# Kernel tuning notes

Measured on AMD Instinct MI355X. Metric: run time of the kernel, lower is better.

## Reference

```python
import jax, jax.numpy as jnp
import numpy as np

TAU_FF = 10
TAU_FB = 10
NB_FF = 8
NB_FB = 1
MU = 0.5
N_IN = 2048
N_HID = 2048
N_OUT = 2048


def raised_cosine_pillow_08(tau, n_basis, mu):
    # Pillow et al. 2008 log-raised-cosine basis; returns [n_basis, tau].
    # Fixed (non-learned) constant in the original module.
    t = jnp.arange(tau, dtype=jnp.float32)
    c = jnp.arange(n_basis, dtype=jnp.float32)
    arg = jnp.clip(mu * jnp.pi * jnp.log1p(t)[None, :] - mu * jnp.pi * c[:, None],
                   -jnp.pi, jnp.pi)
    return 0.5 * (1.0 + jnp.cos(arg))


# transposed like the torch module: [tau, n_basis]
FF_FILT = raised_cosine_pillow_08(TAU_FF, NB_FF, MU).T
FB_FILT = raised_cosine_pillow_08(TAU_FB, NB_FB, MU).T


def _layer_step(inp_hist, spk_hist, ff_w, fb_w, bias, key):
    # inp_hist: [n_in, T]; spk_hist: [n_out, Th]; ff_w: [n_out, n_in, NB_FF]
    T = inp_hist.shape[-1]
    ff_trace = jnp.matmul(inp_hist[..., ::-1], FF_FILT[:T])       # [n_in, NB_FF]
    ff_pot = jnp.einsum('oib,ib->o', ff_w, ff_trace)              # [n_out]
    Th = spk_hist.shape[-1]
    fb_trace = jnp.matmul(spk_hist[:, ::-1], FB_FILT[:Th])        # [n_out, NB_FB]
    fb_pot = jnp.sum(fb_w * fb_trace, axis=-1)                    # [n_out]
    p = jax.nn.sigmoid(ff_pot + fb_pot + bias)
    spikes = jax.random.bernoulli(key, jax.lax.stop_gradient(p)).astype(p.dtype)
    # memory_length (10) > current history width (2), so the update just
    # appends one column (matches torch slice [:, 1-memory_length:]).
    new_hist = jnp.concatenate([spk_hist, spikes[:, None]], axis=-1)
    return p, spikes, new_hist


def setup_inputs() -> dict:
    key = jax.random.key(0)
    ks = jax.random.split(key, 10)

    def xav(k, shape, fan_in, fan_out):
        a = np.sqrt(3.0) * np.sqrt(2.0 / float(fan_in + fan_out))
        return jax.random.uniform(k, shape, jnp.float32, -a, a)

    fi, fo = N_IN * NB_FF, N_HID * NB_FF  # fan of ff_weights [n_out, n_in, nb]
    return {
        'inputs_history': (jax.random.uniform(ks[0], (N_IN, TAU_FF)) < 0.3).astype(jnp.float32),
        'ff_w0': xav(ks[1], (N_HID, N_IN, NB_FF), fi, fo),
        'fb_w0': xav(ks[2], (N_HID, NB_FB), fi, fo),
        'b0': xav(ks[3], (N_HID,), fi, fo),
        'ff_w1': xav(ks[4], (N_HID, N_HID, NB_FF), fi, fo),
        'fb_w1': xav(ks[5], (N_HID, NB_FB), fi, fo),
        'b1': xav(ks[6], (N_HID,), fi, fo),
        'ff_w2': xav(ks[7], (N_OUT, N_HID, NB_FF), fi, fo),
        'fb_w2': xav(ks[8], (N_OUT, NB_FB), fi, fo),
        'b2': xav(ks[9], (N_OUT,), fi, fo),
    }


def reference(inputs_history, ff_w0, fb_w0, b0, ff_w1, fb_w1, b1,
              ff_w2, fb_w2, b2):
    # LayeredSNN.forward with n_samples=1, target=None.
    k0, k1, k2 = jax.random.split(jax.random.key(42), 3)
    h0 = jnp.zeros((N_HID, 2), jnp.float32)   # initial spiking histories
    h1 = jnp.zeros((N_HID, 2), jnp.float32)
    h2 = jnp.zeros((N_OUT, 2), jnp.float32)
    p0, s0, h0 = _layer_step(inputs_history, h0, ff_w0, fb_w0, b0, k0)
    p1, s1, h1 = _layer_step(h0, h1, ff_w1, fb_w1, b1, k1)   # reads updated h0
    p2, s2, h2 = _layer_step(h1, h2, ff_w2, fb_w2, b2, k2)   # out layer
    net_probas = p2[None]                      # [1, n_out]
    net_outputs = s2[None]                     # [1, n_out]
    probas_hidden = jnp.stack([p0, p1])[None]  # [1, n_hidden_layers, n_hid]
    outputs_hidden = jnp.stack([s0, s1])[None]
    return net_probas, net_outputs, probas_hidden, outputs_hidden
```

## Files before the change

kernel.cpp:

```cpp
#include <hip/hip_runtime.h>
#include <hip/hip_bf16.h>
#include <stdint.h>
#include <stddef.h>

#define WS_F_OFF      64
#define WS_TRACE0_OFF 768
#define WS_S0_OFF     131840
#define WS_S1_OFF     148224

__host__ __device__ inline void tf2x32(uint32_t k0, uint32_t k1,
                                       uint32_t& x0, uint32_t& x1) {
  uint32_t ks0 = k0, ks1 = k1, ks2 = k0 ^ k1 ^ 0x1BD11BDAu;
  x0 += ks0; x1 += ks1;
#define TF_ROT(v, n) (((v) << (n)) | ((v) >> (32 - (n))))
#define TF_R(r) { x0 += x1; x1 = TF_ROT(x1, r); x1 ^= x0; }
  TF_R(13) TF_R(15) TF_R(26) TF_R(6)   x0 += ks1; x1 += ks2 + 1u;
  TF_R(17) TF_R(29) TF_R(16) TF_R(24)  x0 += ks2; x1 += ks0 + 2u;
  TF_R(13) TF_R(15) TF_R(26) TF_R(6)   x0 += ks0; x1 += ks1 + 3u;
  TF_R(17) TF_R(29) TF_R(16) TF_R(24)  x0 += ks1; x1 += ks2 + 4u;
  TF_R(13) TF_R(15) TF_R(26) TF_R(6)   x0 += ks2; x1 += ks0 + 5u;
#undef TF_R
#undef TF_ROT
}

__device__ inline double bf2d(unsigned short b) {
  return (double)__uint_as_float(((uint32_t)b) << 16);
}
__device__ inline unsigned short f2bf(float f) {
  uint32_t u = __float_as_uint(f);
  u += 0x7FFFu + ((u >> 16) & 1u);
  return (unsigned short)(u >> 16);
}

__global__ void snn_init_kernel(const uint32_t* __restrict__ x_words,
                                uint8_t* __restrict__ ws) {
  uint32_t* flag = (uint32_t*)ws;
  double* F = (double*)(ws + WS_F_OFF);
  int t = threadIdx.x;
  if (t == 0) {
    int cnt = 0;
    for (int k = 0; k < 256; ++k) {
      uint32_t w = x_words[k];
      cnt += (w == 0u || w == 0x3F800000u) ? 1 : 0;
    }
    *flag = (cnt == 256) ? 0u : 1u;
  }
  if (t < 80) {
    int tt = t >> 3, b = t & 7;
    const double PI = 3.14159265358979311599796346854;
    double arg = 0.5 * PI * log1p((double)tt) - 0.5 * PI * (double)b;
    arg = fmin(fmax(arg, -PI), PI);
    F[t] = 0.5 * (1.0 + cos(arg));
  }
}

__global__ void snn_trace0_kernel(const void* __restrict__ X,
                                  uint8_t* __restrict__ ws) {
  const uint32_t flag = *(const uint32_t*)ws;
  const double* F = (const double*)(ws + WS_F_OFF);
  double* tr = (double*)(ws + WS_TRACE0_OFF);
  int idx = blockIdx.x * blockDim.x + threadIdx.x;
  if (idx >= 2048 * 8) return;
  int i = idx >> 3, b = idx & 7;
  double acc = 0.0;
  if (flag) {
    const unsigned short* Xb = (const unsigned short*)X;
    #pragma unroll
    for (int t = 0; t < 10; ++t) acc += bf2d(Xb[i * 10 + (9 - t)]) * F[t * 8 + b];
  } else {
    const float* Xf = (const float*)X;
    #pragma unroll
    for (int t = 0; t < 10; ++t) acc += (double)Xf[i * 10 + (9 - t)] * F[t * 8 + b];
  }
  tr[idx] = acc;
}

__global__ __launch_bounds__(256) void snn_layer_kernel(
    const void* __restrict__ W, const void* __restrict__ bias,
    uint8_t* __restrict__ ws,
    int traceMode,
    const double* __restrict__ sPrev,
    double* __restrict__ sOutD,
    uint32_t key0, uint32_t key1,
    void* __restrict__ out, int pOff, int sOff)
{
  const uint32_t flag = *(const uint32_t*)ws;
  const double* F = (const double*)(ws + WS_F_OFF);
  const double* tr0 = (const double*)(ws + WS_TRACE0_OFF);
  const int o = blockIdx.x;
  const int tid = threadIdx.x;
  double acc = 0.0;

  if (traceMode == 0) {
    if (flag) {
      const unsigned short* Wrow = (const unsigned short*)W + (size_t)o * 16384;
      for (int i = tid; i < 2048; i += 256) {
        uint4 v = *(const uint4*)(Wrow + i * 8);
        const double* tr = tr0 + i * 8;
        acc += bf2d((unsigned short)(v.x & 0xFFFFu)) * tr[0]
             + bf2d((unsigned short)(v.x >> 16))     * tr[1]
             + bf2d((unsigned short)(v.y & 0xFFFFu)) * tr[2]
             + bf2d((unsigned short)(v.y >> 16))     * tr[3]
             + bf2d((unsigned short)(v.z & 0xFFFFu)) * tr[4]
             + bf2d((unsigned short)(v.z >> 16))     * tr[5]
             + bf2d((unsigned short)(v.w & 0xFFFFu)) * tr[6]
             + bf2d((unsigned short)(v.w >> 16))     * tr[7];
      }
    } else {
      const float* Wrow = (const float*)W + (size_t)o * 16384;
      for (int i = tid; i < 2048; i += 256) {
        float4 a = *(const float4*)(Wrow + i * 8);
        float4 b = *(const float4*)(Wrow + i * 8 + 4);
        const double* tr = tr0 + i * 8;
        acc += (double)a.x * tr[0] + (double)a.y * tr[1]
             + (double)a.z * tr[2] + (double)a.w * tr[3]
             + (double)b.x * tr[4] + (double)b.y * tr[5]
             + (double)b.z * tr[6] + (double)b.w * tr[7];
      }
    }
  } else {
    double F0[8];
    #pragma unroll
    for (int b = 0; b < 8; ++b) F0[b] = F[b];
    if (flag) {
      const unsigned short* Wrow = (const unsigned short*)W + (size_t)o * 16384;
      for (int i = tid; i < 2048; i += 256) {
        double si = sPrev[i];
        uint4 v = *(const uint4*)(Wrow + i * 8);
        double dot = bf2d((unsigned short)(v.x & 0xFFFFu)) * F0[0]
                   + bf2d((unsigned short)(v.x >> 16))     * F0[1]
                   + bf2d((unsigned short)(v.y & 0xFFFFu)) * F0[2]
                   + bf2d((unsigned short)(v.y >> 16))     * F0[3]
                   + bf2d((unsigned short)(v.z & 0xFFFFu)) * F0[4]
                   + bf2d((unsigned short)(v.z >> 16))     * F0[5]
                   + bf2d((unsigned short)(v.w & 0xFFFFu)) * F0[6]
                   + bf2d((unsigned short)(v.w >> 16))     * F0[7];
        acc += si * dot;
      }
    } else {
      const float* Wrow = (const float*)W + (size_t)o * 16384;
      for (int i = tid; i < 2048; i += 256) {
        double si = sPrev[i];
        float4 a = *(const float4*)(Wrow + i * 8);
        float4 b = *(const float4*)(Wrow + i * 8 + 4);
        double dot = (double)a.x * F0[0] + (double)a.y * F0[1]
                   + (double)a.z * F0[2] + (double)a.w * F0[3]
                   + (double)b.x * F0[4] + (double)b.y * F0[5]
                   + (double)b.z * F0[6] + (double)b.w * F0[7];
        acc += si * dot;
      }
    }
  }

  __shared__ double red[256];
  red[tid] = acc;
  __syncthreads();
  for (int s = 128; s > 0; s >>= 1) {
    if (tid < s) red[tid] += red[tid + s];
    __syncthreads();
  }

  if (tid == 0) {
    double bb = flag ? bf2d(((const unsigned short*)bias)[o])
                     : (double)((const float*)bias)[o];
    double x = red[0] + bb;
    double p = 1.0 / (1.0 + exp(-x));
    uint32_t x0 = 0u, x1 = (uint32_t)o;
    tf2x32(key0, key1, x0, x1);
    uint32_t wbits = x0 ^ x1;
    float u = __uint_as_float((wbits >> 9) | 0x3F800000u) - 1.0f;
    double s = ((double)u < p) ? 1.0 : 0.0;
    if (flag) {
      unsigned short* ob = (unsigned short*)out;
      ob[pOff + o] = f2bf((float)p);
      ob[sOff + o] = f2bf((float)s);
    } else {
      float* of = (float*)out;
      of[pOff + o] = (float)p;
      of[sOff + o] = (float)s;
    }
    if (sOutD) sOutD[o] = s;
  }
}

extern "C" void kernel_launch(void* const* d_in, const int* in_sizes, int n_in,
                              void* d_out, int out_size, void* d_ws, size_t ws_size,
                              hipStream_t stream) {
  uint32_t k0a = 0u, k0b = 0u;  tf2x32(0u, 42u, k0a, k0b);
  uint32_t k1a = 0u, k1b = 1u;  tf2x32(0u, 42u, k1a, k1b);
  uint32_t k2a = 0u, k2b = 2u;  tf2x32(0u, 42u, k2a, k2b);

  uint8_t* ws = (uint8_t*)d_ws;
  double* s0d = (double*)(ws + WS_S0_OFF);
  double* s1d = (double*)(ws + WS_S1_OFF);

  snn_init_kernel<<<1, 128, 0, stream>>>((const uint32_t*)d_in[0], ws);
  snn_trace0_kernel<<<64, 256, 0, stream>>>(d_in[0], ws);
  snn_layer_kernel<<<2048, 256, 0, stream>>>(d_in[1], d_in[3], ws, 0, nullptr, s0d,
                                             k0a, k0b, d_out, 4096, 8192);
  snn_layer_kernel<<<2048, 256, 0, stream>>>(d_in[4], d_in[6], ws, 1, s0d, s1d,
                                             k1a, k1b, d_out, 6144, 10240);
  snn_layer_kernel<<<2048, 256, 0, stream>>>(d_in[7], d_in[9], ws, 1, s1d, nullptr,
                                             k2a, k2b, d_out, 0, 2048);
}
```

Baseline: 387.1 us.

## Assign one wavefront per output row and fuse init with trace kernel

```diff
diff --git a/kernel.cpp b/kernel.cpp
--- a/kernel.cpp
+++ b/kernel.cpp
@@ -32,52 +32,57 @@
   return (unsigned short)(u >> 16);
 }
 
-__global__ void snn_init_kernel(const uint32_t* __restrict__ x_words,
-                                uint8_t* __restrict__ ws) {
-  uint32_t* flag = (uint32_t*)ws;
-  double* F = (double*)(ws + WS_F_OFF);
-  int t = threadIdx.x;
-  if (t == 0) {
-    int cnt = 0;
-    for (int k = 0; k < 256; ++k) {
-      uint32_t w = x_words[k];
-      cnt += (w == 0u || w == 0x3F800000u) ? 1 : 0;
-    }
-    *flag = (cnt == 256) ? 0u : 1u;
-  }
-  if (t < 80) {
-    int tt = t >> 3, b = t & 7;
+__global__ __launch_bounds__(256) void snn_prep_kernel(
+    const void* __restrict__ X, uint8_t* __restrict__ ws) {
+  __shared__ unsigned long long smask[4];
+  __shared__ double sF[80];
+  __shared__ int s_flag;
+  const int tid = threadIdx.x;
+
+  const uint32_t* xw = (const uint32_t*)X;
+  uint32_t w = xw[tid];
+  bool ok = (w == 0u || w == 0x3F800000u);
+  unsigned long long m = __ballot(ok);
+  if ((tid & 63) == 0) smask[tid >> 6] = m;
+
+  if (tid < 80) {
+    int tt = tid >> 3, b = tid & 7;
     const double PI = 3.14159265358979311599796346854;
     double arg = 0.5 * PI * log1p((double)tt) - 0.5 * PI * (double)b;
     arg = fmin(fmax(arg, -PI), PI);
-    F[t] = 0.5 * (1.0 + cos(arg));
-  }
-}
-
-__global__ void snn_trace0_kernel(const void* __restrict__ X,
-                                  uint8_t* __restrict__ ws) {
-  const uint32_t flag = *(const uint32_t*)ws;
-  const double* F = (const double*)(ws + WS_F_OFF);
-  double* tr = (double*)(ws + WS_TRACE0_OFF);
-  int idx = blockIdx.x * blockDim.x + threadIdx.x;
-  if (idx >= 2048 * 8) return;
-  int i = idx >> 3, b = idx & 7;
+    sF[tid] = 0.5 * (1.0 + cos(arg));
+  }
+  __syncthreads();
+  if (tid == 0) {
+    bool allbin = ((smask[0] & smask[1] & smask[2] & smask[3]) == ~0ull);
+    s_flag = allbin ? 0 : 1;
+  }
+  __syncthreads();
+  const int flag = s_flag;
+
+  if (blockIdx.x == 0) {
+    if (tid == 0) *(uint32_t*)ws = (uint32_t)flag;
+    if (tid < 80) ((double*)(ws + WS_F_OFF))[tid] = sF[tid];
+  }
+
+  const int idx = blockIdx.x * 256 + tid;
+  const int i = idx >> 3, b = idx & 7;
   double acc = 0.0;
   if (flag) {
     const unsigned short* Xb = (const unsigned short*)X;
     #pragma unroll
-    for (int t = 0; t < 10; ++t) acc += bf2d(Xb[i * 10 + (9 - t)]) * F[t * 8 + b];
+    for (int t = 0; t < 10; ++t) acc += bf2d(Xb[i * 10 + (9 - t)]) * sF[t * 8 + b];
   } else {
     const float* Xf = (const float*)X;
     #pragma unroll
-    for (int t = 0; t < 10; ++t) acc += (double)Xf[i * 10 + (9 - t)] * F[t * 8 + b];
-  }
-  tr[idx] = acc;
+    for (int t = 0; t < 10; ++t) acc += (double)Xf[i * 10 + (9 - t)] * sF[t * 8 + b];
+  }
+  ((double*)(ws + WS_TRACE0_OFF))[idx] = acc;
 }
 
 __global__ __launch_bounds__(256) void snn_layer_kernel(
     const void* __restrict__ W, const void* __restrict__ bias,
-    uint8_t* __restrict__ ws,
+    const uint8_t* __restrict__ ws,
     int traceMode,
     const double* __restrict__ sPrev,
     double* __restrict__ sOutD,
@@ -87,35 +92,42 @@
   const uint32_t flag = *(const uint32_t*)ws;
   const double* F = (const double*)(ws + WS_F_OFF);
   const double* tr0 = (const double*)(ws + WS_TRACE0_OFF);
-  const int o = blockIdx.x;
-  const int tid = threadIdx.x;
-  double acc = 0.0;
+  const int lane = threadIdx.x & 63;
+  const int row = blockIdx.x * 4 + (threadIdx.x >> 6);
+
+  double acc[8];
+  #pragma unroll
+  for (int b = 0; b < 8; ++b) acc[b] = 0.0;
 
   if (traceMode == 0) {
     if (flag) {
-      const unsigned short* Wrow = (const unsigned short*)W + (size_t)o * 16384;
-      for (int i = tid; i < 2048; i += 256) {
-        uint4 v = *(const uint4*)(Wrow + i * 8);
-        const double* tr = tr0 + i * 8;
-        acc += bf2d((unsigned short)(v.x & 0xFFFFu)) * tr[0]
-             + bf2d((unsigned short)(v.x >> 16))     * tr[1]
-             + bf2d((unsigned short)(v.y & 0xFFFFu)) * tr[2]
-             + bf2d((unsigned short)(v.y >> 16))     * tr[3]
-             + bf2d((unsigned short)(v.z & 0xFFFFu)) * tr[4]
-             + bf2d((unsigned short)(v.z >> 16))     * tr[5]
-             + bf2d((unsigned short)(v.w & 0xFFFFu)) * tr[6]
-             + bf2d((unsigned short)(v.w >> 16))     * tr[7];
+      const unsigned short* Wr = (const unsigned short*)W + (size_t)row * 16384;
+      for (int s = 0; s < 32; ++s) {
+        int i = s * 64 + lane;
+        uint4 v = *(const uint4*)(Wr + i * 8);
+        const double2* t = (const double2*)(tr0 + i * 8);
+        double2 t0 = t[0], t1 = t[1], t2 = t[2], t3 = t[3];
+        acc[0] += bf2d((unsigned short)(v.x & 0xFFFFu)) * t0.x;
+        acc[1] += bf2d((unsigned short)(v.x >> 16))     * t0.y;
+        acc[2] += bf2d((unsigned short)(v.y & 0xFFFFu)) * t1.x;
+        acc[3] += bf2d((unsigned short)(v.y >> 16))     * t1.y;
+        acc[4] += bf2d((unsigned short)(v.z & 0xFFFFu)) * t2.x;
+        acc[5] += bf2d((unsigned short)(v.z >> 16))     * t2.y;
+        acc[6] += bf2d((unsigned short)(v.w & 0xFFFFu)) * t3.x;
+        acc[7] += bf2d((unsigned short)(v.w >> 16))     * t3.y;
       }
     } else {
-      const float* Wrow = (const float*)W + (size_t)o * 16384;
-      for (int i = tid; i < 2048; i += 256) {
-        float4 a = *(const float4*)(Wrow + i * 8);
-        float4 b = *(const float4*)(Wrow + i * 8 + 4);
-        const double* tr = tr0 + i * 8;
-        acc += (double)a.x * tr[0] + (double)a.y * tr[1]
-             + (double)a.z * tr[2] + (double)a.w * tr[3]
-             + (double)b.x * tr[4] + (double)b.y * tr[5]
-             + (double)b.z * tr[6] + (double)b.w * tr[7];
+      const float* Wr = (const float*)W + (size_t)row * 16384;
+      for (int s = 0; s < 32; ++s) {
+        int i = s * 64 + lane;
+        float4 a = *(const float4*)(Wr + i * 8);
+        float4 c = *(const float4*)(Wr + i * 8 + 4);
+        const double2* t = (const double2*)(tr0 + i * 8);
+        double2 t0 = t[0], t1 = t[1], t2 = t[2], t3 = t[3];
+        acc[0] += (double)a.x * t0.x;  acc[1] += (double)a.y * t0.y;
+        acc[2] += (double)a.z * t1.x;  acc[3] += (double)a.w * t1.y;
+        acc[4] += (double)c.x * t2.x;  acc[5] += (double)c.y * t2.y;
+        acc[6] += (double)c.z * t3.x;  acc[7] += (double)c.w * t3.y;
       }
     }
   } else {
@@ -123,63 +135,64 @@
     #pragma unroll
     for (int b = 0; b < 8; ++b) F0[b] = F[b];
     if (flag) {
-      const unsigned short* Wrow = (const unsigned short*)W + (size_t)o * 16384;
-      for (int i = tid; i < 2048; i += 256) {
+      const unsigned short* Wr = (const unsigned short*)W + (size_t)row * 16384;
+      for (int s = 0; s < 32; ++s) {
+        int i = s * 64 + lane;
+        uint4 v = *(const uint4*)(Wr + i * 8);
         double si = sPrev[i];
-        uint4 v = *(const uint4*)(Wrow + i * 8);
-        double dot = bf2d((unsigned short)(v.x & 0xFFFFu)) * F0[0]
-                   + bf2d((unsigned short)(v.x >> 16))     * F0[1]
-                   + bf2d((unsigned short)(v.y & 0xFFFFu)) * F0[2]
-                   + bf2d((unsigned short)(v.y >> 16))     * F0[3]
-                   + bf2d((unsigned short)(v.z & 0xFFFFu)) * F0[4]
-                   + bf2d((unsigned short)(v.z >> 16))     * F0[5]
-                   + bf2d((unsigned short)(v.w & 0xFFFFu)) * F0[6]
-                   + bf2d((unsigned short)(v.w >> 16))     * F0[7];
-        acc += si * dot;
+        acc[0] += (bf2d((unsigned short)(v.x & 0xFFFFu)) * F0[0]) * si;
+        acc[1] += (bf2d((unsigned short)(v.x >> 16))     * F0[1]) * si;
+        acc[2] += (bf2d((unsigned short)(v.y & 0xFFFFu)) * F0[2]) * si;
+        acc[3] += (bf2d((unsigned short)(v.y >> 16))     * F0[3]) * si;
+        acc[4] += (bf2d((unsigned short)(v.z & 0xFFFFu)) * F0[4]) * si;
+        acc[5] += (bf2d((unsigned short)(v.z >> 16))     * F0[5]) * si;
+        acc[6] += (bf2d((unsigned short)(v.w & 0xFFFFu)) * F0[6]) * si;
+        acc[7] += (bf2d((unsigned short)(v.w >> 16))     * F0[7]) * si;
       }
     } else {
-      const float* Wrow = (const float*)W + (size_t)o * 16384;
-      for (int i = tid; i < 2048; i += 256) {
+      const float* Wr = (const float*)W + (size_t)row * 16384;
+      for (int s = 0; s < 32; ++s) {
+        int i = s * 64 + lane;
+        float4 a = *(const float4*)(Wr + i * 8);
+        float4 c = *(const float4*)(Wr + i * 8 + 4);
         double si = sPrev[i];
-        float4 a = *(const float4*)(Wrow + i * 8);
-        float4 b = *(const float4*)(Wrow + i * 8 + 4);
-        double dot = (double)a.x * F0[0] + (double)a.y * F0[1]
-                   + (double)a.z * F0[2] + (double)a.w * F0[3]
-                   + (double)b.x * F0[4] + (double)b.y * F0[5]
-                   + (double)b.z * F0[6] + (double)b.w * F0[7];
-        acc += si * dot;
+        acc[0] += ((double)a.x * F0[0]) * si;
+        acc[1] += ((double)a.y * F0[1]) * si;
+        acc[2] += ((double)a.z * F0[2]) * si;
+        acc[3] += ((double)a.w * F0[3]) * si;
+        acc[4] += ((double)c.x * F0[4]) * si;
+        acc[5] += ((double)c.y * F0[5]) * si;
+        acc[6] += ((double)c.z * F0[6]) * si;
+        acc[7] += ((double)c.w * F0[7]) * si;
       }
     }
   }
 
-  __shared__ double red[256];
-  red[tid] = acc;
-  __syncthreads();
-  for (int s = 128; s > 0; s >>= 1) {
-    if (tid < s) red[tid] += red[tid + s];
-    __syncthreads();
-  }
-
-  if (tid == 0) {
-    double bb = flag ? bf2d(((const unsigned short*)bias)[o])
-                     : (double)((const float*)bias)[o];
-    double x = red[0] + bb;
+  double r = ((acc[0] + acc[1]) + (acc[2] + acc[3])) +
+             ((acc[4] + acc[5]) + (acc[6] + acc[7]));
+  #pragma unroll
+  for (int off = 32; off > 0; off >>= 1) r += __shfl_down(r, off, 64);
+
+  if (lane == 0) {
+    double bb = flag ? bf2d(((const unsigned short*)bias)[row])
+                     : (double)((const float*)bias)[row];
+    double x = r + bb;
     double p = 1.0 / (1.0 + exp(-x));
-    uint32_t x0 = 0u, x1 = (uint32_t)o;
+    uint32_t x0 = 0u, x1 = (uint32_t)row;
     tf2x32(key0, key1, x0, x1);
     uint32_t wbits = x0 ^ x1;
     float u = __uint_as_float((wbits >> 9) | 0x3F800000u) - 1.0f;
-    double s = ((double)u < p) ? 1.0 : 0.0;
+    double sp = ((double)u < p) ? 1.0 : 0.0;
     if (flag) {
       unsigned short* ob = (unsigned short*)out;
-      ob[pOff + o] = f2bf((float)p);
-      ob[sOff + o] = f2bf((float)s);
+      ob[pOff + row] = f2bf((float)p);
+      ob[sOff + row] = f2bf((float)sp);
     } else {
       float* of = (float*)out;
-      of[pOff + o] = (float)p;
-      of[sOff + o] = (float)s;
+      of[pOff + row] = (float)p;
+      of[sOff + row] = (float)sp;
     }
-    if (sOutD) sOutD[o] = s;
+    if (sOutD) sOutD[row] = sp;
   }
 }
 
@@ -194,12 +207,11 @@
   double* s0d = (double*)(ws + WS_S0_OFF);
   double* s1d = (double*)(ws + WS_S1_OFF);
 
-  snn_init_kernel<<<1, 128, 0, stream>>>((const uint32_t*)d_in[0], ws);
-  snn_trace0_kernel<<<64, 256, 0, stream>>>(d_in[0], ws);
-  snn_layer_kernel<<<2048, 256, 0, stream>>>(d_in[1], d_in[3], ws, 0, nullptr, s0d,
-                                             k0a, k0b, d_out, 4096, 8192);
-  snn_layer_kernel<<<2048, 256, 0, stream>>>(d_in[4], d_in[6], ws, 1, s0d, s1d,
-                                             k1a, k1b, d_out, 6144, 10240);
-  snn_layer_kernel<<<2048, 256, 0, stream>>>(d_in[7], d_in[9], ws, 1, s1d, nullptr,
-                                             k2a, k2b, d_out, 0, 2048);
-}
+  snn_prep_kernel<<<64, 256, 0, stream>>>(d_in[0], ws);
+  snn_layer_kernel<<<512, 256, 0, stream>>>(d_in[1], d_in[3], ws, 0, nullptr, s0d,
+                                            k0a, k0b, d_out, 4096, 8192);
+  snn_layer_kernel<<<512, 256, 0, stream>>>(d_in[4], d_in[6], ws, 1, s0d, s1d,
+                                            k1a, k1b, d_out, 6144, 10240);
+  snn_layer_kernel<<<512, 256, 0, stream>>>(d_in[7], d_in[9], ws, 1, s1d, nullptr,
+                                            k2a, k2b, d_out, 0, 2048);
+}
```

After: 376.5 us. 1.03x faster.
